# Kernel tuning notes

Measured on AMD Instinct MI355X. Metric: run time of the kernel, lower is better.

The kernel has to match this reference:

```python
import jax, jax.numpy as jnp
import numpy as np

B, S, H = 64, 512, 768
BETA = 1.0
SENT_W, TOK_W, REG_W = 1.0, 1.0, 0.01


def setup_inputs() -> dict:
    key = jax.random.key(0)
    ks = jax.random.split(key, 8)
    hidden_states = jax.random.normal(ks[0], (B, S, H), dtype=jnp.float32)
    # offset_mapping[:,:,0] != 0 marks continuation subwords; position 0 is always a word start
    is_cont = jax.random.bernoulli(ks[1], 0.3, (B, S)).astype(jnp.int32)
    is_cont = is_cont.at[:, 0].set(0)
    offset_mapping = jnp.stack([is_cont, jnp.zeros((B, S), jnp.int32)], axis=-1)
    labels = jax.random.randint(ks[2], (B, S), 0, 2, dtype=jnp.int32)
    std = 0.02
    w1 = jax.random.normal(ks[3], (H, 100), jnp.float32) * std
    b1 = jnp.zeros((100,), jnp.float32)
    w2 = jax.random.normal(ks[4], (100, 1), jnp.float32) * std
    b2 = jnp.zeros((1,), jnp.float32)
    sw1 = jax.random.normal(ks[5], (H, 300), jnp.float32) * std
    sb1 = jnp.zeros((300,), jnp.float32)
    sw2 = jax.random.normal(ks[6], (300, 1), jnp.float32) * std
    sb2 = jnp.zeros((1,), jnp.float32)
    return dict(hidden_states=hidden_states, offset_mapping=offset_mapping, labels=labels,
                w1=w1, b1=b1, w2=w2, b2=b2, sw1=sw1, sb1=sb1, sw2=sw2, sb2=sb2)


def reference(hidden_states, offset_mapping, labels, w1, b1, w2, b2, sw1, sb1, sw2, sb2):
    b, s, h = hidden_states.shape
    # token attention head: Linear -> tanh -> Linear -> sigmoid, squeeze last dim
    tok = jax.nn.sigmoid(jnp.tanh(hidden_states @ w1 + b1) @ w2 + b2)[..., 0]  # [B,S]
    # vectorized segmented max over subword groups (replaces the python loop):
    # each word = a start position (offset[...,0]==0) plus following continuations.
    is_start = offset_mapping[:, :, 0] == 0  # [B,S]
    word_id = jnp.cumsum(is_start.astype(jnp.int32), axis=1) - 1  # per-row word index
    seg = (jnp.arange(b, dtype=jnp.int32)[:, None] * s + word_id).reshape(-1)  # global segment id
    segmax = jax.ops.segment_max(tok.reshape(-1), seg, num_segments=b * s)
    word_att = jnp.where(is_start, segmax[seg].reshape(b, s), tok)
    labf = labels.astype(tok.dtype)
    token_attention_mask = ((labels == 0) | (labels == 1)).astype(tok.dtype) * is_start.astype(tok.dtype)
    masked = word_att * token_attention_mask  # token_logits
    pw = jnp.power(masked, BETA)
    norm = pw / jnp.sum(pw, axis=1, keepdims=True)
    pooled = jnp.einsum('bsh,bs->bh', hidden_states, norm)  # bmm(hidden^T, att)
    sent = jax.nn.sigmoid(jnp.tanh(pooled @ sw1 + sb1) @ sw2 + sb2)  # [B,1] sequence_logits
    sentence_labels = jnp.max(labf, axis=1, keepdims=True)
    sentence_loss = jnp.sum((sent - sentence_labels) ** 2)
    zero_labels = jnp.where(labf == 1.0, labf, jnp.zeros_like(labf))
    token_loss = jnp.sum((masked - zero_labels) ** 2)
    ones_mask = jnp.where(masked == 0.0, jnp.ones_like(masked), masked)
    reg_a = jnp.sum(jnp.min(ones_mask, axis=1, keepdims=True) ** 2)
    reg_b = jnp.sum((jnp.max(masked, axis=1, keepdims=True) - sentence_labels) ** 2)
    loss = SENT_W * sentence_loss + TOK_W * token_loss + REG_W * (reg_a + reg_b)
    return loss, sentence_loss, token_loss, reg_a, reg_b, masked, sent
```

## Files before the change

### kernel.cpp

```cpp
#include <hip/hip_runtime.h>
#include <math.h>

#define BB   64
#define SS   512
#define HH   768
#define NU   100
#define NUP  112
#define NT   7
#define KS   24
#define NS1  300
#define MM   (BB*SS)
#define PCH  16
#define PTOK (SS/PCH)

typedef __attribute__((ext_vector_type(8))) short short8;
typedef __attribute__((ext_vector_type(4))) float f32x4;

__device__ __forceinline__ unsigned short f2bf(float x) {
    unsigned int u = __float_as_uint(x);
    u = (u + 0x7FFFu + ((u >> 16) & 1u)) >> 16;
    return (unsigned short)u;
}

__device__ __forceinline__ float tanh_fast(float x) {
    float e = __expf(2.0f * x);
    return 1.0f - 2.0f / (e + 1.0f);
}

__device__ __forceinline__ float sigmoid_fast(float z) {
    return 1.0f / (1.0f + __expf(-z));
}

__global__ __launch_bounds__(64) void repack_kernel(
    const float* __restrict__ w1,
    const float* __restrict__ b1,
    const float* __restrict__ w2,
    unsigned short* __restrict__ Bp,
    float* __restrict__ b1p, float* __restrict__ w2p,
    float* __restrict__ accs)
{
    const int n  = blockIdx.x / KS;
    const int ks = blockIdx.x - n * KS;
    const int l  = threadIdx.x;
    const int c  = l & 15, g = l >> 4;
    const int u  = n * 16 + c;

    unsigned int w[4];
#pragma unroll
    for (int jp = 0; jp < 4; jp++) {
        unsigned int lo, hi;
        {
            int k = ks * 32 + g * 8 + jp * 2;
            float x = (u < NU) ? w1[(size_t)k * NU + u] : 0.0f;
            lo = f2bf(x);
        }
        {
            int k = ks * 32 + g * 8 + jp * 2 + 1;
            float x = (u < NU) ? w1[(size_t)k * NU + u] : 0.0f;
            hi = f2bf(x);
        }
        w[jp] = lo | (hi << 16);
    }
    uint4* dst = (uint4*)(Bp + ((size_t)(n * KS + ks) * 64 + l) * 8);
    *dst = make_uint4(w[0], w[1], w[2], w[3]);

    if (blockIdx.x == 0) {
        for (int i = l; i < NUP; i += 64) {
            b1p[i] = (i < NU) ? b1[i] : 0.0f;
            w2p[i] = (i < NU) ? w2[i] : 0.0f;
        }
        if (l < 8) accs[l] = 0.0f;
    }
}

__global__ __launch_bounds__(256) void tok_mlp_mfma(
    const float* __restrict__ hs,
    const unsigned short* __restrict__ Bp,
    const float* __restrict__ b1p,
    const float* __restrict__ w2p,
    const float* __restrict__ b2,
    float* __restrict__ tok)
{
    const int tid = threadIdx.x;
    const int wv = tid >> 6, l = tid & 63;
    const int c = l & 15, g = l >> 4;
    const int m0 = blockIdx.x * 64 + wv * 16;

    f32x4 acc[NT];
#pragma unroll
    for (int n = 0; n < NT; n++) acc[n] = (f32x4){0.f, 0.f, 0.f, 0.f};

    const float* arow = hs + (size_t)(m0 + c) * HH + g * 8;
    const unsigned short* bbase = Bp + (size_t)l * 8;

    float4 a0 = *(const float4*)(arow);
    float4 a1 = *(const float4*)(arow + 4);

    for (int ks = 0; ks < KS; ks++) {
        float4 n0 = a0, n1 = a1;
        if (ks + 1 < KS) {
            n0 = *(const float4*)(arow + (ks + 1) * 32);
            n1 = *(const float4*)(arow + (ks + 1) * 32 + 4);
        }
        short8 af;
        af[0] = (short)f2bf(a0.x); af[1] = (short)f2bf(a0.y);
        af[2] = (short)f2bf(a0.z); af[3] = (short)f2bf(a0.w);
        af[4] = (short)f2bf(a1.x); af[5] = (short)f2bf(a1.y);
        af[6] = (short)f2bf(a1.z); af[7] = (short)f2bf(a1.w);
#pragma unroll
        for (int n = 0; n < NT; n++) {
            short8 bf = *(const short8*)(bbase + (size_t)(n * KS + ks) * 64 * 8);
            acc[n] = __builtin_amdgcn_mfma_f32_16x16x32_bf16(af, bf, acc[n], 0, 0, 0);
        }
        a0 = n0; a1 = n1;
    }

    float p[4];
#pragma unroll
    for (int j = 0; j < 4; j++) {
        float s = 0.0f;
#pragma unroll
        for (int n = 0; n < NT; n++) {
            int u = n * 16 + c;
            s += tanh_fast(acc[n][j] + b1p[u]) * w2p[u];
        }
        p[j] = s;
    }
#pragma unroll
    for (int off = 1; off < 16; off <<= 1) {
#pragma unroll
        for (int j = 0; j < 4; j++) p[j] += __shfl_xor(p[j], off, 64);
    }
    if (c == 0) {
        float bias = b2[0];
#pragma unroll
        for (int j = 0; j < 4; j++) {
            float z = p[j] + bias;
            tok[m0 + g * 4 + j] = sigmoid_fast(z);
        }
    }
}

__global__ __launch_bounds__(256) void row_kernel(
    const float* __restrict__ tok,
    const int*   __restrict__ offset,
    const int*   __restrict__ labels,
    float* __restrict__ masked_out,
    float* __restrict__ rowsum,
    float* __restrict__ rowmax,
    float* __restrict__ rowmin,
    float* __restrict__ sentlab,
    float* __restrict__ accs)
{
    __shared__ float tokL[SS];
    __shared__ float maskedL[SS];
    __shared__ int   startL[SS];
    __shared__ int   labL[SS];
    __shared__ float wredA[4][5];

    const int b = blockIdx.x, tid = threadIdx.x;

    for (int s = tid; s < SS; s += 256) {
        tokL[s]   = tok[b * SS + s];
        startL[s] = (offset[(size_t)(b * SS + s) * 2] == 0) ? 1 : 0;
        labL[s]   = labels[b * SS + s];
    }
    __syncthreads();

    for (int s = tid; s < SS; s += 256) {
        float w;
        if (startL[s]) {
            float m = tokL[s];
            for (int j = s + 1; j < SS && !startL[j]; j++) m = fmaxf(m, tokL[j]);
            w = m;
        } else {
            w = tokL[s];
        }
        int lab = labL[s];
        float maskv = (((lab == 0) || (lab == 1)) && startL[s]) ? 1.0f : 0.0f;
        float mk = w * maskv;
        maskedL[s] = mk;
        masked_out[b * SS + s] = mk;
    }
    __syncthreads();

    float psum = 0.0f, pmax = -INFINITY, pmin = INFINITY, pml = 0.0f, ploss = 0.0f;
    for (int s = tid; s < SS; s += 256) {
        float mk = maskedL[s];
        psum += mk;
        pmax = fmaxf(pmax, mk);
        float ones = (mk == 0.0f) ? 1.0f : mk;
        pmin = fminf(pmin, ones);
        float lf = (float)labL[s];
        pml = fmaxf(pml, lf);
        float zl = (lf == 1.0f) ? lf : 0.0f;
        float d = mk - zl;
        ploss += d * d;
    }
#pragma unroll
    for (int off = 32; off >= 1; off >>= 1) {
        psum  += __shfl_xor(psum, off, 64);
        pmax   = fmaxf(pmax, __shfl_xor(pmax, off, 64));
        pmin   = fminf(pmin, __shfl_xor(pmin, off, 64));
        pml    = fmaxf(pml,  __shfl_xor(pml, off, 64));
        ploss += __shfl_xor(ploss, off, 64);
    }
    const int wv = tid >> 6, ln = tid & 63;
    if (ln == 0) {
        wredA[wv][0] = psum; wredA[wv][1] = pmax; wredA[wv][2] = pmin;
        wredA[wv][3] = pml;  wredA[wv][4] = ploss;
    }
    __syncthreads();
    if (tid == 0) {
        float s = 0.0f, mx = -INFINITY, mn = INFINITY, ml = 0.0f, ls = 0.0f;
        for (int w = 0; w < 4; w++) {
            s += wredA[w][0];
            mx = fmaxf(mx, wredA[w][1]);
            mn = fminf(mn, wredA[w][2]);
            ml = fmaxf(ml, wredA[w][3]);
            ls += wredA[w][4];
        }
        rowsum[b] = s; rowmax[b] = mx; rowmin[b] = mn; sentlab[b] = ml;
        atomicAdd(&accs[0], ls);
    }
}

__global__ __launch_bounds__(192) void pool_partial_kernel(
    const float* __restrict__ hs,
    const float* __restrict__ masked,
    const float* __restrict__ rowsum,
    float* __restrict__ pp)
{
    __shared__ float normL[PTOK];
    __shared__ float normC[PTOK];
    __shared__ int   idxC[PTOK];
    __shared__ int   cntS;
    const int b = blockIdx.x >> 4, p = blockIdx.x & 15;
    const int tid = threadIdx.x;
    const float inv = 1.0f / rowsum[b];
    if (tid < PTOK) normL[tid] = masked[b * SS + p * PTOK + tid] * inv;
    __syncthreads();
    if (tid == 0) {
        int c = 0;
        for (int s = 0; s < PTOK; s++) {
            float v = normL[s];
            if (v != 0.0f) { idxC[c] = s; normC[c] = v; c++; }
        }
        cntS = c;
    }
    __syncthreads();
    const int cnt = cntS;

    float4 a = make_float4(0.f, 0.f, 0.f, 0.f);
    const float* hb = hs + (size_t)b * SS * HH + (size_t)p * PTOK * HH;
#pragma unroll 2
    for (int i = 0; i < cnt; i++) {
        float w = normC[i];
        float4 v = *(const float4*)(hb + (size_t)idxC[i] * HH + tid * 4);
        a.x += v.x * w; a.y += v.y * w; a.z += v.z * w; a.w += v.w * w;
    }
    *(float4*)(pp + (size_t)(b * PCH + p) * HH + tid * 4) = a;
}

__global__ __launch_bounds__(256) void sent_kernel(
    const float* __restrict__ pp,
    const float* __restrict__ sw1,
    const float* __restrict__ sb1,
    const float* __restrict__ sw2,
    const float* __restrict__ sb2,
    const float* __restrict__ rowmax,
    const float* __restrict__ rowmin,
    const float* __restrict__ sentlab,
    float* __restrict__ sent_out,
    float* __restrict__ accs,
    float* __restrict__ out)
{
    __shared__ float pooledL[HH];
    __shared__ float t1L[NS1];
    __shared__ float wredB[4];

    const int b = blockIdx.x, tid = threadIdx.x;
#pragma unroll
    for (int j = 0; j < 3; j++) {
        int h = tid + j * 256;
        float s = 0.0f;
#pragma unroll
        for (int p = 0; p < PCH; p++) s += pp[(size_t)(b * PCH + p) * HH + h];
        pooledL[h] = s;
    }
    __syncthreads();

    for (int u = tid; u < NS1; u += 256) {
        float y = sb1[u];
        for (int h = 0; h < HH; h++) y += pooledL[h] * sw1[(size_t)h * NS1 + u];
        t1L[u] = tanh_fast(y);
    }
    __syncthreads();

    float z = 0.0f;
    for (int u = tid; u < NS1; u += 256) z += t1L[u] * sw2[u];
#pragma unroll
    for (int off = 32; off >= 1; off >>= 1) z += __shfl_xor(z, off, 64);
    const int wv = tid >> 6, ln = tid & 63;
    if (ln == 0) wredB[wv] = z;
    __syncthreads();
    if (tid == 0) {
        float zz = wredB[0] + wredB[1] + wredB[2] + wredB[3] + sb2[0];
        float sentv = sigmoid_fast(zz);
        sent_out[b] = sentv;
        float sl = sentlab[b];
        float ds = sentv - sl;
        atomicAdd(&accs[1], ds * ds);
        float dm = rowmax[b] - sl;
        atomicAdd(&accs[3], dm * dm);
        atomicAdd(&accs[2], rowmin[b] * rowmin[b]);

        __threadfence();
        int* ticket = (int*)(accs + 4);
        int old = atomicAdd(ticket, 1);
        if (old == BB - 1) {
            float tokl  = atomicAdd(&accs[0], 0.0f);
            float sentl = atomicAdd(&accs[1], 0.0f);
            float rega  = atomicAdd(&accs[2], 0.0f);
            float regb  = atomicAdd(&accs[3], 0.0f);
            out[0] = sentl + tokl + 0.01f * (rega + regb);
            out[1] = sentl;
            out[2] = tokl;
            out[3] = rega;
            out[4] = regb;
        }
    }
}

extern "C" void kernel_launch(void* const* d_in, const int* in_sizes, int n_in,
                              void* d_out, int out_size, void* d_ws, size_t ws_size,
                              hipStream_t stream)
{
    const float* hs     = (const float*)d_in[0];
    const int*   offm   = (const int*)  d_in[1];
    const int*   labels = (const int*)  d_in[2];
    const float* w1     = (const float*)d_in[3];
    const float* b1     = (const float*)d_in[4];
    const float* w2     = (const float*)d_in[5];
    const float* b2     = (const float*)d_in[6];
    const float* sw1    = (const float*)d_in[7];
    const float* sb1    = (const float*)d_in[8];
    const float* sw2    = (const float*)d_in[9];
    const float* sb2    = (const float*)d_in[10];

    float* out     = (float*)d_out;
    float* maskedO = out + 5;
    float* sentO   = out + 5 + MM;

    float* ws      = (float*)d_ws;
    float* tok     = ws;
    float* pp      = ws + MM;
    float* rowsum  = pp + (size_t)BB * PCH * HH;
    float* rowmax  = rowsum + BB;
    float* rowmin  = rowmax + BB;
    float* sentlab = rowmin + BB;
    float* accs    = sentlab + BB;
    float* b1p     = accs + 8;
    float* w2p     = b1p + NUP;
    size_t ofs = (size_t)((w2p + NUP) - ws);
    ofs = (ofs + 3) & ~(size_t)3;
    unsigned short* Bp = (unsigned short*)(ws + ofs);

    repack_kernel<<<NT * KS, 64, 0, stream>>>(w1, b1, w2, Bp, b1p, w2p, accs);
    tok_mlp_mfma<<<MM / 64, 256, 0, stream>>>(hs, Bp, b1p, w2p, b2, tok);
    row_kernel<<<BB, 256, 0, stream>>>(tok, offm, labels, maskedO,
                                       rowsum, rowmax, rowmin, sentlab, accs);
    pool_partial_kernel<<<BB * PCH, 192, 0, stream>>>(hs, maskedO, rowsum, pp);
    sent_kernel<<<BB, 256, 0, stream>>>(pp, sw1, sb1, sw2, sb2,
                                        rowmax, rowmin, sentlab, sentO, accs, out);
}
```

Baseline: 255.0 us.

## Split sentence MLP across blocks with transposed sw1 and warp-level dot products

```diff
diff --git a/kernel.cpp b/kernel.cpp
--- a/kernel.cpp
+++ b/kernel.cpp
@@ -12,6 +12,8 @@
 #define MM   (BB*SS)
 #define PCH  16
 #define PTOK (SS/PCH)
+#define UB   5
+#define UPW  15
 
 typedef __attribute__((ext_vector_type(8))) short short8;
 typedef __attribute__((ext_vector_type(4))) float f32x4;
@@ -35,41 +37,58 @@
     const float* __restrict__ w1,
     const float* __restrict__ b1,
     const float* __restrict__ w2,
+    const float* __restrict__ sw1,
     unsigned short* __restrict__ Bp,
     float* __restrict__ b1p, float* __restrict__ w2p,
-    float* __restrict__ accs)
-{
-    const int n  = blockIdx.x / KS;
-    const int ks = blockIdx.x - n * KS;
-    const int l  = threadIdx.x;
-    const int c  = l & 15, g = l >> 4;
-    const int u  = n * 16 + c;
-
-    unsigned int w[4];
-#pragma unroll
-    for (int jp = 0; jp < 4; jp++) {
-        unsigned int lo, hi;
-        {
-            int k = ks * 32 + g * 8 + jp * 2;
-            float x = (u < NU) ? w1[(size_t)k * NU + u] : 0.0f;
-            lo = f2bf(x);
-        }
-        {
-            int k = ks * 32 + g * 8 + jp * 2 + 1;
-            float x = (u < NU) ? w1[(size_t)k * NU + u] : 0.0f;
-            hi = f2bf(x);
-        }
-        w[jp] = lo | (hi << 16);
-    }
-    uint4* dst = (uint4*)(Bp + ((size_t)(n * KS + ks) * 64 + l) * 8);
-    *dst = make_uint4(w[0], w[1], w[2], w[3]);
-
-    if (blockIdx.x == 0) {
-        for (int i = l; i < NUP; i += 64) {
-            b1p[i] = (i < NU) ? b1[i] : 0.0f;
-            w2p[i] = (i < NU) ? w2[i] : 0.0f;
-        }
-        if (l < 8) accs[l] = 0.0f;
+    float* __restrict__ sw1T,
+    float* __restrict__ accs,
+    float* __restrict__ zacc,
+    int*   __restrict__ btick)
+{
+    const int blk = blockIdx.x;
+    const int l   = threadIdx.x;
+
+    if (blk < NT * KS) {
+        const int n  = blk / KS;
+        const int ks = blk - n * KS;
+        const int c  = l & 15, g = l >> 4;
+        const int u  = n * 16 + c;
+
+        unsigned int w[4];
+#pragma unroll
+        for (int jp = 0; jp < 4; jp++) {
+            unsigned int lo, hi;
+            {
+                int k = ks * 32 + g * 8 + jp * 2;
+                float x = (u < NU) ? w1[(size_t)k * NU + u] : 0.0f;
+                lo = f2bf(x);
+            }
+            {
+                int k = ks * 32 + g * 8 + jp * 2 + 1;
+                float x = (u < NU) ? w1[(size_t)k * NU + u] : 0.0f;
+                hi = f2bf(x);
+            }
+            w[jp] = lo | (hi << 16);
+        }
+        uint4* dst = (uint4*)(Bp + ((size_t)(n * KS + ks) * 64 + l) * 8);
+        *dst = make_uint4(w[0], w[1], w[2], w[3]);
+
+        if (blk == 0) {
+            for (int i = l; i < NUP; i += 64) {
+                b1p[i] = (i < NU) ? b1[i] : 0.0f;
+                w2p[i] = (i < NU) ? w2[i] : 0.0f;
+            }
+            if (l < 8) accs[l] = 0.0f;
+            zacc[l]  = 0.0f;
+            btick[l] = 0;
+        }
+    } else {
+        const int u = blk - NT * KS;
+#pragma unroll
+        for (int k = 0; k < HH / 64; k++) {
+            int h = k * 64 + l;
+            sw1T[(size_t)u * HH + h] = sw1[(size_t)h * NS1 + u];
+        }
     }
 }
 
@@ -264,7 +283,7 @@
 
 __global__ __launch_bounds__(256) void sent_kernel(
     const float* __restrict__ pp,
-    const float* __restrict__ sw1,
+    const float* __restrict__ sw1T,
     const float* __restrict__ sb1,
     const float* __restrict__ sw2,
     const float* __restrict__ sb2,
@@ -273,61 +292,77 @@
     const float* __restrict__ sentlab,
     float* __restrict__ sent_out,
     float* __restrict__ accs,
+    float* __restrict__ zacc,
+    int*   __restrict__ btick,
     float* __restrict__ out)
 {
     __shared__ float pooledL[HH];
-    __shared__ float t1L[NS1];
-    __shared__ float wredB[4];
-
-    const int b = blockIdx.x, tid = threadIdx.x;
-#pragma unroll
-    for (int j = 0; j < 3; j++) {
-        int h = tid + j * 256;
+    __shared__ float wzL[4];
+
+    const int b = blockIdx.x / UB, ub = blockIdx.x - b * UB;
+    const int tid = threadIdx.x;
+
+    if (tid < 192) {
+        float4 s = make_float4(0.f, 0.f, 0.f, 0.f);
+        const float* base = pp + (size_t)b * PCH * HH + tid * 4;
+#pragma unroll
+        for (int p = 0; p < PCH; p++) {
+            float4 v = *(const float4*)(base + (size_t)p * HH);
+            s.x += v.x; s.y += v.y; s.z += v.z; s.w += v.w;
+        }
+        *(float4*)(&pooledL[tid * 4]) = s;
+    }
+    __syncthreads();
+
+    const int wv = tid >> 6, l = tid & 63;
+    float zp = 0.0f;
+#pragma unroll
+    for (int i = 0; i < UPW; i++) {
+        const int u = ub * (4 * UPW) + wv * UPW + i;
+        const float* r = sw1T + (size_t)u * HH;
         float s = 0.0f;
 #pragma unroll
-        for (int p = 0; p < PCH; p++) s += pp[(size_t)(b * PCH + p) * HH + h];
-        pooledL[h] = s;
-    }
-    __syncthreads();
-
-    for (int u = tid; u < NS1; u += 256) {
-        float y = sb1[u];
-        for (int h = 0; h < HH; h++) y += pooledL[h] * sw1[(size_t)h * NS1 + u];
-        t1L[u] = tanh_fast(y);
-    }
-    __syncthreads();
-
-    float z = 0.0f;
-    for (int u = tid; u < NS1; u += 256) z += t1L[u] * sw2[u];
-#pragma unroll
-    for (int off = 32; off >= 1; off >>= 1) z += __shfl_xor(z, off, 64);
-    const int wv = tid >> 6, ln = tid & 63;
-    if (ln == 0) wredB[wv] = z;
-    __syncthreads();
+        for (int k = 0; k < 3; k++) {
+            float4 v  = *(const float4*)(r + (k * 64 + l) * 4);
+            float4 pv = *(const float4*)(&pooledL[(k * 64 + l) * 4]);
+            s += v.x * pv.x + v.y * pv.y + v.z * pv.z + v.w * pv.w;
+        }
+#pragma unroll
+        for (int off = 32; off >= 1; off >>= 1) s += __shfl_xor(s, off, 64);
+        zp += tanh_fast(s + sb1[u]) * sw2[u];
+    }
+    if (l == 0) wzL[wv] = zp;
+    __syncthreads();
+
     if (tid == 0) {
-        float zz = wredB[0] + wredB[1] + wredB[2] + wredB[3] + sb2[0];
-        float sentv = sigmoid_fast(zz);
-        sent_out[b] = sentv;
-        float sl = sentlab[b];
-        float ds = sentv - sl;
-        atomicAdd(&accs[1], ds * ds);
-        float dm = rowmax[b] - sl;
-        atomicAdd(&accs[3], dm * dm);
-        atomicAdd(&accs[2], rowmin[b] * rowmin[b]);
-
+        float blockz = wzL[0] + wzL[1] + wzL[2] + wzL[3];
+        atomicAdd(&zacc[b], blockz);
         __threadfence();
-        int* ticket = (int*)(accs + 4);
-        int old = atomicAdd(ticket, 1);
-        if (old == BB - 1) {
-            float tokl  = atomicAdd(&accs[0], 0.0f);
-            float sentl = atomicAdd(&accs[1], 0.0f);
-            float rega  = atomicAdd(&accs[2], 0.0f);
-            float regb  = atomicAdd(&accs[3], 0.0f);
-            out[0] = sentl + tokl + 0.01f * (rega + regb);
-            out[1] = sentl;
-            out[2] = tokl;
-            out[3] = rega;
-            out[4] = regb;
+        int old = atomicAdd(&btick[b], 1);
+        if (old == UB - 1) {
+            float z = atomicAdd(&zacc[b], 0.0f) + sb2[0];
+            float sentv = sigmoid_fast(z);
+            sent_out[b] = sentv;
+            float sl = sentlab[b];
+            float ds = sentv - sl;
+            atomicAdd(&accs[1], ds * ds);
+            float dm = rowmax[b] - sl;
+            atomicAdd(&accs[3], dm * dm);
+            atomicAdd(&accs[2], rowmin[b] * rowmin[b]);
+            __threadfence();
+            int* t2 = (int*)(accs + 4);
+            int o2 = atomicAdd(t2, 1);
+            if (o2 == BB - 1) {
+                float tokl  = atomicAdd(&accs[0], 0.0f);
+                float sentl = atomicAdd(&accs[1], 0.0f);
+                float rega  = atomicAdd(&accs[2], 0.0f);
+                float regb  = atomicAdd(&accs[3], 0.0f);
+                out[0] = sentl + tokl + 0.01f * (rega + regb);
+                out[1] = sentl;
+                out[2] = tokl;
+                out[3] = rega;
+                out[4] = regb;
+            }
         }
     }
 }
@@ -360,17 +395,22 @@
     float* rowmin  = rowmax + BB;
     float* sentlab = rowmin + BB;
     float* accs    = sentlab + BB;
-    float* b1p     = accs + 8;
+    float* zacc    = accs + 8;
+    float* btickf  = zacc + BB;
+    float* b1p     = btickf + BB;
     float* w2p     = b1p + NUP;
-    size_t ofs = (size_t)((w2p + NUP) - ws);
+    float* sw1T    = w2p + NUP;
+    size_t ofs = (size_t)((sw1T + (size_t)NS1 * HH) - ws);
     ofs = (ofs + 3) & ~(size_t)3;
     unsigned short* Bp = (unsigned short*)(ws + ofs);
 
-    repack_kernel<<<NT * KS, 64, 0, stream>>>(w1, b1, w2, Bp, b1p, w2p, accs);
+    repack_kernel<<<NT * KS + NS1, 64, 0, stream>>>(w1, b1, w2, sw1, Bp, b1p, w2p,
+                                                    sw1T, accs, zacc, (int*)btickf);
     tok_mlp_mfma<<<MM / 64, 256, 0, stream>>>(hs, Bp, b1p, w2p, b2, tok);
     row_kernel<<<BB, 256, 0, stream>>>(tok, offm, labels, maskedO,
                                        rowsum, rowmax, rowmin, sentlab, accs);
     pool_partial_kernel<<<BB * PCH, 192, 0, stream>>>(hs, maskedO, rowsum, pp);
-    sent_kernel<<<BB, 256, 0, stream>>>(pp, sw1, sb1, sw2, sb2,
-                                        rowmax, rowmin, sentlab, sentO, accs, out);
-}
+    sent_kernel<<<BB * UB, 256, 0, stream>>>(pp, sw1T, sb1, sw2, sb2,
+                                             rowmax, rowmin, sentlab, sentO,
+                                             accs, zacc, (int*)btickf, out);
+}
```

Measured after the change: 214.7 us. 1.19x faster.
